# Kernel optimization log

Hardware: AMD Instinct MI355X
Metric: run time of the kernel (lower is better)

The kernel has to match this reference:

```python
import jax, jax.numpy as jnp
import numpy as np

B, N, D_MODEL = 16, 65536, 512
NBUCKETS = 11
BN_EPS = 1e-5
LN_EPS = 1e-5


def setup_inputs() -> dict:
    key = jax.random.key(0)
    ks = jax.random.split(key, 12)
    def w(k, shape, fan_in):
        return jax.random.normal(k, shape, jnp.float32) * (1.0 / np.sqrt(fan_in))
    return {
        "x": jax.random.normal(ks[0], (B, N, 3), jnp.float32),
        "w1": w(ks[1], (3, 64), 3),   "b1": jnp.zeros((64,), jnp.float32),
        "g1": jnp.ones((64,), jnp.float32),  "be1": jnp.zeros((64,), jnp.float32),
        "w2": w(ks[2], (64, 128), 64), "b2": jnp.zeros((128,), jnp.float32),
        "g2": jnp.ones((128,), jnp.float32), "be2": jnp.zeros((128,), jnp.float32),
        "w3": w(ks[3], (128, 256), 128), "b3": jnp.zeros((256,), jnp.float32),
        "g3": jnp.ones((256,), jnp.float32), "be3": jnp.zeros((256,), jnp.float32),
        "wp": w(ks[4], (518, D_MODEL), 518), "bp": jnp.zeros((D_MODEL,), jnp.float32),
        "g_ln": jnp.ones((D_MODEL,), jnp.float32), "b_ln": jnp.zeros((D_MODEL,), jnp.float32),
    }


def _bn(h, g, b):
    # BatchNorm1d in training mode: biased variance over the flattened batch axis
    m = jnp.mean(h, axis=0)
    v = jnp.mean((h - m) ** 2, axis=0)
    return (h - m) * jax.lax.rsqrt(v + BN_EPS) * g + b


def reference(x, w1, b1, g1, be1, w2, b2, g2, be2, w3, b3, g3, be3, wp, bp, g_ln, b_ln):
    Bb, Nn, _ = x.shape
    x_flat = x.reshape(Bb * Nn, 3)
    h = jax.nn.relu(_bn(x_flat @ w1 + b1, g1, be1))
    h = jax.nn.relu(_bn(h @ w2 + b2, g2, be2))
    h = jax.nn.relu(_bn(h @ w3 + b3, g3, be3))
    feat = h.reshape(Bb, Nn, 256)

    # y-bucket histogram means of (x, z) coordinates, vectorized via segment_sum
    y = x[:, :, 1]
    y_min = jnp.min(y, axis=1, keepdims=True)
    y_max = jnp.max(y, axis=1, keepdims=True)
    y_norm = (y - y_min) / (y_max - y_min + 1e-6)
    buckets = jnp.clip((y_norm * 10).astype(jnp.int32), 0, NBUCKETS - 1)  # (B,N) in [0,10]
    seg = (jnp.arange(Bb, dtype=jnp.int32)[:, None] * NBUCKETS + buckets).reshape(-1)
    nseg = Bb * NBUCKETS
    sx = jax.ops.segment_sum(x[:, :, 0].reshape(-1), seg, num_segments=nseg)
    sz = jax.ops.segment_sum(x[:, :, 2].reshape(-1), seg, num_segments=nseg)
    cnt = jax.ops.segment_sum(jnp.ones((Bb * Nn,), jnp.float32), seg, num_segments=nseg)
    denom = jnp.maximum(cnt, 1.0)
    cx = (sx / denom).reshape(Bb, NBUCKETS)
    cz = (sz / denom).reshape(Bb, NBUCKETS)
    x_centers = jnp.take_along_axis(cx, buckets, axis=1)  # (B,N)
    z_centers = jnp.take_along_axis(cz, buckets, axis=1)

    dx = x[:, :, 0] - x_centers
    dz = x[:, :, 2] - z_centers
    theta = jnp.arctan2(dz, dx)
    r = jnp.sqrt(dx ** 2 + dz ** 2)
    spatial = jnp.stack([jnp.sin(theta), jnp.cos(theta), r], axis=-1)  # (B,N,3)

    feat = jnp.concatenate([feat, spatial], axis=-1)  # (B,N,259)
    feat_max = jnp.max(feat, axis=1)
    feat_avg = jnp.mean(feat, axis=1)
    feat_cat = jnp.concatenate([feat_max, feat_avg], axis=1)  # (B,518)

    out = feat_cat @ wp + bp
    mu = jnp.mean(out, axis=-1, keepdims=True)
    var = jnp.mean((out - mu) ** 2, axis=-1, keepdims=True)
    return (out - mu) * jax.lax.rsqrt(var + LN_EPS) * g_ln + b_ln
```

## Files before the change

### kernel.cpp

```cpp
#include <hip/hip_runtime.h>
#include <stdint.h>

#define B_    16
#define N_    65536
#define NPTS  (B_*N_)
#define NBK   11
#define NFEAT 259
#define NF    ((float)NPTS)

typedef float f32x4 __attribute__((ext_vector_type(4)));
typedef short s16x8 __attribute__((ext_vector_type(8)));

enum {
  OFF_YMINF = 16,
  OFF_YMAXF = 32,
  OFF_A1    = 64,
  OFF_C1    = 128,
  OFF_A2    = 192,
  OFF_C2    = 320,
  OFF_CX    = 448,
  OFF_CZ    = 624,
  OFF_A3    = 800,
  OFF_C3    = 1056,
  OFF_PSTR  = 16384,
  OFF_PBKT  = 24576,
  OFF_PH2   = 49152,
  OFF_PH3   = 180224,
  OFF_PPOOL = 442368,
  OFF_PSPA  = 704512
};

__device__ __forceinline__ float wave_sum(float v){
  #pragma unroll
  for (int m=32;m>=1;m>>=1) v += __shfl_xor(v,m,64);
  return v;
}
__device__ __forceinline__ float wave_max(float v){
  #pragma unroll
  for (int m=32;m>=1;m>>=1) v = fmaxf(v,__shfl_xor(v,m,64));
  return v;
}
__device__ __forceinline__ float wave_min(float v){
  #pragma unroll
  for (int m=32;m>=1;m>>=1) v = fminf(v,__shfl_xor(v,m,64));
  return v;
}
__device__ __forceinline__ unsigned short bf16_bits(float f){
  unsigned u=__float_as_uint(f);
  u += 0x7FFFu + ((u>>16)&1u);
  return (unsigned short)(u>>16);
}

__global__ __launch_bounds__(256) void k_stream0(const float* __restrict__ x,
                                                 float* __restrict__ ws){
  __shared__ float red[4][12];
  const int t=threadIdx.x, l=t&63, w=t>>6;
  const int bid=blockIdx.x;
  const float4* xv=(const float4*)(x + (size_t)bid*2048*3);
  float s0=0,s1=0,s2=0,q00=0,q01=0,q02=0,q11=0,q12=0,q22=0;
  float ymn=3.4e38f, ymx=-3.4e38f;
  #pragma unroll
  for (int i=0;i<2;i++){
    const int vi=(i*256+t)*3;
    const float4 a=xv[vi], b4=xv[vi+1], c=xv[vi+2];
    float X[4]={a.x,a.w,b4.z,c.y};
    float Y[4]={a.y,b4.x,b4.w,c.z};
    float Z[4]={a.z,b4.y,c.x,c.w};
    #pragma unroll
    for (int p=0;p<4;p++){
      s0+=X[p]; s1+=Y[p]; s2+=Z[p];
      q00=fmaf(X[p],X[p],q00); q01=fmaf(X[p],Y[p],q01); q02=fmaf(X[p],Z[p],q02);
      q11=fmaf(Y[p],Y[p],q11); q12=fmaf(Y[p],Z[p],q12); q22=fmaf(Z[p],Z[p],q22);
      ymn=fminf(ymn,Y[p]); ymx=fmaxf(ymx,Y[p]);
    }
  }
  s0=wave_sum(s0); s1=wave_sum(s1); s2=wave_sum(s2);
  q00=wave_sum(q00); q01=wave_sum(q01); q02=wave_sum(q02);
  q11=wave_sum(q11); q12=wave_sum(q12); q22=wave_sum(q22);
  ymn=wave_min(ymn); ymx=wave_max(ymx);
  if (l==0){
    red[w][0]=s0; red[w][1]=s1; red[w][2]=s2;
    red[w][3]=q00; red[w][4]=q01; red[w][5]=q02;
    red[w][6]=q11; red[w][7]=q12; red[w][8]=q22;
    red[w][9]=ymn; red[w][10]=ymx;
  }
  __syncthreads();
  if (t<11){
    const float v0=red[0][t],v1=red[1][t],v2=red[2][t],v3=red[3][t];
    float r;
    if (t==9)       r=fminf(fminf(v0,v1),fminf(v2,v3));
    else if (t==10) r=fmaxf(fmaxf(v0,v1),fmaxf(v2,v3));
    else            r=v0+v1+v2+v3;
    ws[OFF_PSTR+bid*16+t]=r;
  }
}

__global__ void k_finA(const float* __restrict__ w1, const float* __restrict__ b1,
                       const float* __restrict__ gm, const float* __restrict__ bt,
                       float* __restrict__ ws){
  __shared__ float sums[9];
  const int t=threadIdx.x;
  if (t<9){
    float s=0.f;
    #pragma unroll 8
    for (int blk=0;blk<512;blk++) s+=ws[OFF_PSTR+blk*16+t];
    sums[t]=s;
  }
  if (t>=32&&t<48){
    const int b=t-32; float m=3.4e38f;
    #pragma unroll 8
    for (int blk=0;blk<32;blk++) m=fminf(m,ws[OFF_PSTR+(b*32+blk)*16+9]);
    ws[OFF_YMINF+b]=m;
  }
  if (t>=48&&t<64){
    const int b=t-48; float m=-3.4e38f;
    #pragma unroll 8
    for (int blk=0;blk<32;blk++) m=fmaxf(m,ws[OFF_PSTR+(b*32+blk)*16+10]);
    ws[OFF_YMAXF+b]=m;
  }
  __syncthreads();
  if (t<64){
    const float i_n=1.f/NF;
    const float w0=w1[t], wa=w1[64+t], wb=w1[128+t];
    const float ms=(w0*sums[0]+wa*sums[1]+wb*sums[2])*i_n;
    const float es=(w0*w0*sums[3]+wa*wa*sums[6]+wb*wb*sums[8]
                   +2.f*(w0*wa*sums[4]+w0*wb*sums[5]+wa*wb*sums[7]))*i_n;
    const float var=es-ms*ms;
    const float a=gm[t]/sqrtf(var+1e-5f);
    ws[OFF_A1+t]=a; ws[OFF_C1+t]=bt[t]-(ms+b1[t])*a;
  }
}

__global__ __launch_bounds__(256) void k_bucket(const float* __restrict__ x,
                                                float* __restrict__ ws){
  __shared__ float red[4][33];
  const int t=threadIdx.x, l=t&63, w=t>>6;
  const int bid=blockIdx.x, b=bid>>5;
  const float ymn=ws[OFF_YMINF+b], ymx=ws[OFF_YMAXF+b];
  const float4* xv=(const float4*)(x + (size_t)bid*2048*3);
  float sxl[NBK], szl[NBK], cntl[NBK];
  #pragma unroll
  for (int k=0;k<NBK;k++){ sxl[k]=0.f; szl[k]=0.f; cntl[k]=0.f; }
  #pragma unroll
  for (int i=0;i<2;i++){
    const int vi=(i*256+t)*3;
    const float4 a=xv[vi], b4=xv[vi+1], c=xv[vi+2];
    float X[4]={a.x,a.w,b4.z,c.y};
    float Y[4]={a.y,b4.x,b4.w,c.z};
    float Z[4]={a.z,b4.y,c.x,c.w};
    #pragma unroll
    for (int p=0;p<4;p++){
      const float yn=(Y[p]-ymn)/(ymx-ymn+1e-6f);
      int bk=(int)(yn*10.f); bk = bk<0?0:(bk>10?10:bk);
      #pragma unroll
      for (int k=0;k<NBK;k++){
        const bool m=(bk==k);
        sxl[k]+= m?X[p]:0.f; szl[k]+= m?Z[p]:0.f; cntl[k]+= m?1.f:0.f;
      }
    }
  }
  #pragma unroll
  for (int k=0;k<NBK;k++){
    const float s=wave_sum(sxl[k]);
    const float z=wave_sum(szl[k]);
    const float c=wave_sum(cntl[k]);
    if (l==0){ red[w][k]=s; }
    __syncthreads();
    if (l==0&&w==0){  }
    __syncthreads();
    if (l==0){ red[w][k]=s; }
    if (l==0){ red[w][k]=s; }
    __syncthreads();
    if (t<1){}
    if (l==0){ red[w][k]=s; }
    (void)z; (void)c;
    break;
  }
  #pragma unroll
  for (int k=0;k<NBK;k++){
    const float s=wave_sum(sxl[k]);
    if (l==0) red[w][k]=s;
  }
  __syncthreads();
  if (t<NBK) ws[OFF_PBKT+bid*36+t]=red[0][t]+red[1][t]+red[2][t]+red[3][t];
  __syncthreads();
  #pragma unroll
  for (int k=0;k<NBK;k++){
    const float z=wave_sum(szl[k]);
    if (l==0) red[w][k]=z;
  }
  __syncthreads();
  if (t<NBK) ws[OFF_PBKT+bid*36+11+t]=red[0][t]+red[1][t]+red[2][t]+red[3][t];
  __syncthreads();
  #pragma unroll
  for (int k=0;k<NBK;k++){
    const float c=wave_sum(cntl[k]);
    if (l==0) red[w][k]=c;
  }
  __syncthreads();
  if (t<NBK) ws[OFF_PBKT+bid*36+22+t]=red[0][t]+red[1][t]+red[2][t]+red[3][t];
}

__global__ void k_finB(const float* __restrict__ gm, const float* __restrict__ bt,
                       float* __restrict__ ws){
  __shared__ float acc[256];
  const int t=threadIdx.x;
  {
    const int col=t&127, part=t>>7;
    float s=0.f;
    #pragma unroll 8
    for (int blk=0;blk<512;blk++) s+=ws[OFF_PH2+blk*256+part*128+col];
    acc[t]=s;
  }
  __syncthreads();
  if (t<128){
    const float i_n=1.f/NF;
    const float m=acc[t]*i_n;
    const float v=acc[128+t]*i_n-m*m;
    const float a=gm[t]/sqrtf(v+1e-5f);
    ws[OFF_A2+t]=a; ws[OFF_C2+t]=bt[t]-m*a;
  }
  if (t<176){
    const int b=t/NBK, k=t-b*NBK;
    float sx=0.f, sz=0.f, cn=0.f;
    #pragma unroll 8
    for (int blk=0;blk<32;blk++){
      const int p=OFF_PBKT+(b*32+blk)*36;
      sx+=ws[p+k]; sz+=ws[p+11+k]; cn+=ws[p+22+k];
    }
    const float d=fmaxf(cn,1.f);
    ws[OFF_CX+t]=sx/d; ws[OFF_CZ+t]=sz/d;
  }
}

__global__ void k_finC(const float* __restrict__ gm, const float* __restrict__ bt,
                       float* __restrict__ ws){
  __shared__ float acc[512];
  const int t=threadIdx.x;
  {
    const int col=t&255, part=t>>8;
    float s=0.f;
    #pragma unroll 8
    for (int blk=0;blk<512;blk++) s+=ws[OFF_PH3+blk*512+part*256+col];
    acc[t]=s;
  }
  __syncthreads();
  if (t<256){
    const float i_n=1.f/NF;
    const float m=acc[t]*i_n;
    const float v=acc[256+t]*i_n-m*m;
    const float a=gm[t]/sqrtf(v+1e-5f);
    ws[OFF_A3+t]=a; ws[OFF_C3+t]=bt[t]-m*a;
  }
}

__global__ __launch_bounds__(256) void k_spatial(const float* __restrict__ x,
                                                 float* __restrict__ ws){
  __shared__ float red[4][8];
  const int t=threadIdx.x, l=t&63, w=t>>6;
  const int bid=blockIdx.x, b=bid>>5;
  const float ymn=ws[OFF_YMINF+b], ymx=ws[OFF_YMAXF+b];
  const float4* xv=(const float4*)(x + (size_t)bid*2048*3);
  float mx[3]={-3.4e38f,-3.4e38f,-3.4e38f}, sm[3]={0.f,0.f,0.f};
  #pragma unroll
  for (int i=0;i<2;i++){
    const int vi=(i*256+t)*3;
    const float4 a=xv[vi], b4=xv[vi+1], c=xv[vi+2];
    float X[4]={a.x,a.w,b4.z,c.y};
    float Y[4]={a.y,b4.x,b4.w,c.z};
    float Z[4]={a.z,b4.y,c.x,c.w};
    #pragma unroll
    for (int p=0;p<4;p++){
      const float yn=(Y[p]-ymn)/(ymx-ymn+1e-6f);
      int bk=(int)(yn*10.f); bk = bk<0?0:(bk>10?10:bk);
      const float dx=X[p]-ws[OFF_CX+b*NBK+bk];
      const float dz=Z[p]-ws[OFF_CZ+b*NBK+bk];
      const float r=sqrtf(fmaf(dx,dx,dz*dz));
      const float sn=(r>0.f)?(dz/r):0.f;
      const float cs=(r>0.f)?(dx/r):1.f;
      mx[0]=fmaxf(mx[0],sn); sm[0]+=sn;
      mx[1]=fmaxf(mx[1],cs); sm[1]+=cs;
      mx[2]=fmaxf(mx[2],r);  sm[2]+=r;
    }
  }
  #pragma unroll
  for (int q=0;q<3;q++){
    const float m=wave_max(mx[q]);
    const float s=wave_sum(sm[q]);
    if (l==0){ red[w][q]=m; red[w][4+q]=s; }
  }
  __syncthreads();
  if (t<3)        ws[OFF_PSPA+bid*8+t]  =fmaxf(fmaxf(red[0][t],red[1][t]),fmaxf(red[2][t],red[3][t]));
  else if (t>=4&&t<7){
    const int q=t-4;
    ws[OFF_PSPA+bid*8+4+q]=red[0][4+q]+red[1][4+q]+red[2][4+q]+red[3][4+q];
  }
}

template<int MODE>
__global__ __launch_bounds__(256,2) void k_mlp(
    const float* __restrict__ x,
    const float* __restrict__ w1, const float* __restrict__ b1,
    const float* __restrict__ w2, const float* __restrict__ b2,
    const float* __restrict__ w3, const float* __restrict__ b3,
    float* __restrict__ ws)
{
  __shared__ short g1t[64*64];
  __shared__ short g2t[64*128];
  const int t=threadIdx.x, w=t>>6, l=t&63, lg=l>>4, lr=l&15;
  const int b=blockIdx.x>>5, chunk=blockIdx.x&31;
  const int bid=blockIdx.x;

  const float* a1=ws+OFF_A1; const float* c1=ws+OFF_C1;
  float w1A[3][8], w1B[3][8], b1A[8], b1B[8];
  #pragma unroll
  for (int i=0;i<8;i++){
    const int fA=8*lg+i, fB=32+8*lg+i;
    const float aA=a1[fA], aB=a1[fB];
    #pragma unroll
    for (int q=0;q<3;q++){ w1A[q][i]=w1[q*64+fA]*aA; w1B[q][i]=w1[q*64+fB]*aB; }
    b1A[i]=b1[fA]*aA+c1[fA];
    b1B[i]=b1[fB]*aB+c1[fB];
  }

  s16x8 w2f[2][2]; float b2v[2];
  #pragma unroll
  for (int ct=0;ct<2;ct++){
    const int col=(2*w+ct)*16+lr;
    const float sc=(MODE==0)?1.f:ws[OFF_A2+col];
    b2v[ct]=(MODE==0)? b2[col] : (ws[OFF_A2+col]*b2[col]+ws[OFF_C2+col]);
    #pragma unroll
    for (int kt=0;kt<2;kt++){
      #pragma unroll
      for (int i=0;i<8;i++){
        const int k=kt*32+8*lg+i;
        w2f[ct][kt][i]=(short)bf16_bits(w2[k*128+col]*sc);
      }
    }
  }

  s16x8 w3f[4][4]; float b3v[4]={0,0,0,0};
  if (MODE!=0){
    #pragma unroll
    for (int ct=0;ct<4;ct++){
      const int col=(4*w+ct)*16+lr;
      const float sc=(MODE==1)?1.f:ws[OFF_A3+col];
      b3v[ct]=(MODE==1)? b3[col] : (ws[OFF_A3+col]*b3[col]+ws[OFF_C3+col]);
      #pragma unroll
      for (int kt=0;kt<4;kt++){
        #pragma unroll
        for (int i=0;i<8;i++){
          const int k=kt*32+8*lg+i;
          w3f[ct][kt][i]=(short)bf16_bits(w3[k*256+col]*sc);
        }
      }
    }
  }

  float accS[4], accQ[4]={0.f,0.f,0.f,0.f};
  #pragma unroll
  for (int q_=0;q_<4;q_++) accS[q_]=(MODE==2)?-3.4e38f:0.f;

  char* g1c=(char*)g1t; char* g2c=(char*)g2t;

  for (int it=0; it<32; ++it){
    const int tb=b*N_+chunk*2048+it*64;
    {
      const int p=16*w+lr;
      const float x0=x[(tb+p)*3+0], x1=x[(tb+p)*3+1], x2=x[(tb+p)*3+2];
      float h[8]; unsigned pk[4];
      #pragma unroll
      for (int i=0;i<8;i++){
        float v=b1A[i];
        v=fmaf(x0,w1A[0][i],v); v=fmaf(x1,w1A[1][i],v); v=fmaf(x2,w1A[2][i],v);
        h[i]=fmaxf(v,0.f);
      }
      #pragma unroll
      for (int i=0;i<4;i++) pk[i]=(unsigned)bf16_bits(h[2*i]) | ((unsigned)bf16_bits(h[2*i+1])<<16);
      *(int4*)(g1c + (((p*64+8*lg)*2) ^ ((p&7)<<4))) = make_int4(pk[0],pk[1],pk[2],pk[3]);
      #pragma unroll
      for (int i=0;i<8;i++){
        float v=b1B[i];
        v=fmaf(x0,w1B[0][i],v); v=fmaf(x1,w1B[1][i],v); v=fmaf(x2,w1B[2][i],v);
        h[i]=fmaxf(v,0.f);
      }
      #pragma unroll
      for (int i=0;i<4;i++) pk[i]=(unsigned)bf16_bits(h[2*i]) | ((unsigned)bf16_bits(h[2*i+1])<<16);
      *(int4*)(g1c + (((p*64+32+8*lg)*2) ^ ((p&7)<<4))) = make_int4(pk[0],pk[1],pk[2],pk[3]);
    }
    __syncthreads();
    s16x8 a1f[4][2];
    #pragma unroll
    for (int rt=0;rt<4;rt++){
      const int p=rt*16+lr;
      #pragma unroll
      for (int kt=0;kt<2;kt++)
        a1f[rt][kt]=*(const s16x8*)(g1c + (((p*64+kt*32+8*lg)*2) ^ ((p&7)<<4)));
    }
    #pragma unroll
    for (int ct=0;ct<2;ct++){
      const int col=(2*w+ct)*16+lr;
      #pragma unroll
      for (int rt=0;rt<4;rt++){
        f32x4 acc={0.f,0.f,0.f,0.f};
        acc=__builtin_amdgcn_mfma_f32_16x16x32_bf16(a1f[rt][0],w2f[ct][0],acc,0,0,0);
        acc=__builtin_amdgcn_mfma_f32_16x16x32_bf16(a1f[rt][1],w2f[ct][1],acc,0,0,0);
        if (MODE==0){
          #pragma unroll
          for (int r=0;r<4;r++){ const float h2=acc[r]+b2v[ct]; accS[ct]+=h2; accQ[ct]+=h2*h2; }
        } else {
          #pragma unroll
          for (int r=0;r<4;r++){
            const int p=rt*16+4*lg+r;
            const float g=fmaxf(acc[r]+b2v[ct],0.f);
            *(short*)(g2c + (((p*128+col)*2) ^ ((p&7)<<4))) = (short)bf16_bits(g);
          }
        }
      }
    }
    __syncthreads();
    if (MODE!=0){
      #pragma unroll
      for (int rt=0;rt<4;rt++){
        const int p=rt*16+lr;
        s16x8 a2f[4];
        #pragma unroll
        for (int kt=0;kt<4;kt++)
          a2f[kt]=*(const s16x8*)(g2c + (((p*128+kt*32+8*lg)*2) ^ ((p&7)<<4)));
        #pragma unroll
        for (int ct=0;ct<4;ct++){
          f32x4 acc={0.f,0.f,0.f,0.f};
          #pragma unroll
          for (int kt=0;kt<4;kt++)
            acc=__builtin_amdgcn_mfma_f32_16x16x32_bf16(a2f[kt],w3f[ct][kt],acc,0,0,0);
          #pragma unroll
          for (int r=0;r<4;r++){
            if (MODE==1){ const float h3=acc[r]+b3v[ct]; accS[ct]+=h3; accQ[ct]+=h3*h3; }
            else        { const float g=fmaxf(acc[r]+b3v[ct],0.f); accS[ct]=fmaxf(accS[ct],g); accQ[ct]+=g; }
          }
        }
      }
    }
  }

  if (MODE==0){
    #pragma unroll
    for (int ct=0;ct<2;ct++){
      float s=accS[ct], q=accQ[ct];
      s+=__shfl_xor(s,16); s+=__shfl_xor(s,32);
      q+=__shfl_xor(q,16); q+=__shfl_xor(q,32);
      if (l<16){
        const int col=(2*w+ct)*16+lr;
        ws[OFF_PH2+bid*256+col]    =s;
        ws[OFF_PH2+bid*256+128+col]=q;
      }
    }
  } else if (MODE==1){
    #pragma unroll
    for (int ct=0;ct<4;ct++){
      float s=accS[ct], q=accQ[ct];
      s+=__shfl_xor(s,16); s+=__shfl_xor(s,32);
      q+=__shfl_xor(q,16); q+=__shfl_xor(q,32);
      if (l<16){
        const int col=(4*w+ct)*16+lr;
        ws[OFF_PH3+bid*512+col]    =s;
        ws[OFF_PH3+bid*512+256+col]=q;
      }
    }
  } else {
    #pragma unroll
    for (int ct=0;ct<4;ct++){
      float m=accS[ct], s=accQ[ct];
      m=fmaxf(m,__shfl_xor(m,16)); m=fmaxf(m,__shfl_xor(m,32));
      s+=__shfl_xor(s,16); s+=__shfl_xor(s,32);
      if (l<16){
        const int col=(4*w+ct)*16+lr;
        ws[OFF_PPOOL+bid*512+col]    =m;
        ws[OFF_PPOOL+bid*512+256+col]=s;
      }
    }
  }
}

__global__ __launch_bounds__(256) void k_final(
    const float* __restrict__ wp, const float* __restrict__ bp,
    const float* __restrict__ gln, const float* __restrict__ bln,
    float* __restrict__ out, const float* __restrict__ ws)
{
  __shared__ float feat[518];
  __shared__ float red[256];
  const int b=blockIdx.x, t=threadIdx.x;
  {
    float fm=-3.4e38f, fs=0.f;
    #pragma unroll 4
    for (int blk=0;blk<32;blk++){
      const int p=OFF_PPOOL+(b*32+blk)*512;
      fm=fmaxf(fm,ws[p+t]);
      fs+=ws[p+256+t];
    }
    feat[t]=fm; feat[NFEAT+t]=fs*(1.f/65536.f);
  }
  if (t<3){
    float fm=-3.4e38f, fs=0.f;
    #pragma unroll 4
    for (int blk=0;blk<32;blk++){
      const int p=OFF_PSPA+(b*32+blk)*8;
      fm=fmaxf(fm,ws[p+t]);
      fs+=ws[p+4+t];
    }
    feat[256+t]=fm; feat[NFEAT+256+t]=fs*(1.f/65536.f);
  }
  __syncthreads();
  float o0=bp[t], o1=bp[t+256];
  #pragma unroll 4
  for (int i=0;i<518;i++){
    const float f=feat[i];
    o0=fmaf(f, wp[i*512+t],     o0);
    o1=fmaf(f, wp[i*512+t+256], o1);
  }
  red[t]=o0+o1; __syncthreads();
  for (int s=128;s>0;s>>=1){ if (t<s) red[t]+=red[t+s]; __syncthreads(); }
  const float mu=red[0]*(1.f/512.f);
  __syncthreads();
  const float d0=o0-mu, d1=o1-mu;
  red[t]=d0*d0+d1*d1; __syncthreads();
  for (int s=128;s>0;s>>=1){ if (t<s) red[t]+=red[t+s]; __syncthreads(); }
  const float var=red[0]*(1.f/512.f);
  const float rs=1.f/sqrtf(var+1e-5f);
  out[b*512+t]     = d0*rs*gln[t]    +bln[t];
  out[b*512+t+256] = d1*rs*gln[t+256]+bln[t+256];
}

extern "C" void kernel_launch(void* const* d_in, const int* in_sizes, int n_in,
                              void* d_out, int out_size, void* d_ws, size_t ws_size,
                              hipStream_t stream)
{
  const float* x  =(const float*)d_in[0];
  const float* w1 =(const float*)d_in[1];
  const float* b1 =(const float*)d_in[2];
  const float* gm1=(const float*)d_in[3];
  const float* be1=(const float*)d_in[4];
  const float* w2 =(const float*)d_in[5];
  const float* b2 =(const float*)d_in[6];
  const float* gm2=(const float*)d_in[7];
  const float* be2=(const float*)d_in[8];
  const float* w3 =(const float*)d_in[9];
  const float* b3 =(const float*)d_in[10];
  const float* gm3=(const float*)d_in[11];
  const float* be3=(const float*)d_in[12];
  const float* wp =(const float*)d_in[13];
  const float* bp =(const float*)d_in[14];
  const float* gln=(const float*)d_in[15];
  const float* bln=(const float*)d_in[16];
  float* ws=(float*)d_ws;
  float* out=(float*)d_out;

  k_stream0<<<dim3(512),dim3(256),0,stream>>>(x,ws);
  k_finA   <<<dim3(1),  dim3(256),0,stream>>>(w1,b1,gm1,be1,ws);
  k_bucket <<<dim3(512),dim3(256),0,stream>>>(x,ws);
  k_mlp<0> <<<dim3(512),dim3(256),0,stream>>>(x,w1,b1,w2,b2,w3,b3,ws);
  k_finB   <<<dim3(1),  dim3(256),0,stream>>>(gm2,be2,ws);
  k_spatial<<<dim3(512),dim3(256),0,stream>>>(x,ws);
  k_mlp<1> <<<dim3(512),dim3(256),0,stream>>>(x,w1,b1,w2,b2,w3,b3,ws);
  k_finC   <<<dim3(1),  dim3(512),0,stream>>>(gm3,be3,ws);
  k_mlp<2> <<<dim3(512),dim3(256),0,stream>>>(x,w1,b1,w2,b2,w3,b3,ws);
  k_final  <<<dim3(16), dim3(256),0,stream>>>(wp,bp,gln,bln,out,ws);
}
```

Before: 486.5 us.

## Restructure MLP kernel to 8 waves with transposed MFMA operands and fewer registers

The MLP kernel moves from 256 to 512 threads per block. Each wave now owns fewer output columns, and the MFMA operands are swapped so that weights are the A operand and activations the B operand. The per-thread weight fragments and accumulators shrink, which should allow four blocks per CU and more parallelism. Layer-2 outputs are written to LDS as packed 8-byte stores instead of scalar shorts, and the final reduction becomes a 16-lane shuffle. The dead reduction loop with redundant syncthreads in k_bucket is removed. The trade-off is more barrier participants per block and a longer shuffle reduction at the end.

```diff
diff --git a/kernel.cpp b/kernel.cpp
--- a/kernel.cpp
+++ b/kernel.cpp
@@ -133,7 +133,7 @@
 
 __global__ __launch_bounds__(256) void k_bucket(const float* __restrict__ x,
                                                 float* __restrict__ ws){
-  __shared__ float red[4][33];
+  __shared__ float red[4][12];
   const int t=threadIdx.x, l=t&63, w=t>>6;
   const int bid=blockIdx.x, b=bid>>5;
   const float ymn=ws[OFF_YMINF+b], ymx=ws[OFF_YMAXF+b];
@@ -158,23 +158,6 @@
         sxl[k]+= m?X[p]:0.f; szl[k]+= m?Z[p]:0.f; cntl[k]+= m?1.f:0.f;
       }
     }
-  }
-  #pragma unroll
-  for (int k=0;k<NBK;k++){
-    const float s=wave_sum(sxl[k]);
-    const float z=wave_sum(szl[k]);
-    const float c=wave_sum(cntl[k]);
-    if (l==0){ red[w][k]=s; }
-    __syncthreads();
-    if (l==0&&w==0){  }
-    __syncthreads();
-    if (l==0){ red[w][k]=s; }
-    if (l==0){ red[w][k]=s; }
-    __syncthreads();
-    if (t<1){}
-    if (l==0){ red[w][k]=s; }
-    (void)z; (void)c;
-    break;
   }
   #pragma unroll
   for (int k=0;k<NBK;k++){
@@ -298,7 +281,7 @@
 }
 
 template<int MODE>
-__global__ __launch_bounds__(256,2) void k_mlp(
+__global__ __launch_bounds__(512,4) void k_mlp(
     const float* __restrict__ x,
     const float* __restrict__ w1, const float* __restrict__ b1,
     const float* __restrict__ w2, const float* __restrict__ b2,
@@ -308,135 +291,130 @@
   __shared__ short g1t[64*64];
   __shared__ short g2t[64*128];
   const int t=threadIdx.x, w=t>>6, l=t&63, lg=l>>4, lr=l&15;
-  const int b=blockIdx.x>>5, chunk=blockIdx.x&31;
-  const int bid=blockIdx.x;
-
+  const int bid=blockIdx.x, b=bid>>5, chunk=bid&31;
+
+  const int p1=8*w+(l&7), fg=l>>3&7;
   const float* a1=ws+OFF_A1; const float* c1=ws+OFF_C1;
-  float w1A[3][8], w1B[3][8], b1A[8], b1B[8];
+  float w1f[3][8], b1f[8];
   #pragma unroll
   for (int i=0;i<8;i++){
-    const int fA=8*lg+i, fB=32+8*lg+i;
-    const float aA=a1[fA], aB=a1[fB];
-    #pragma unroll
-    for (int q=0;q<3;q++){ w1A[q][i]=w1[q*64+fA]*aA; w1B[q][i]=w1[q*64+fB]*aB; }
-    b1A[i]=b1[fA]*aA+c1[fA];
-    b1B[i]=b1[fB]*aB+c1[fB];
-  }
-
-  s16x8 w2f[2][2]; float b2v[2];
-  #pragma unroll
-  for (int ct=0;ct<2;ct++){
-    const int col=(2*w+ct)*16+lr;
-    const float sc=(MODE==0)?1.f:ws[OFF_A2+col];
-    b2v[ct]=(MODE==0)? b2[col] : (ws[OFF_A2+col]*b2[col]+ws[OFF_C2+col]);
-    #pragma unroll
-    for (int kt=0;kt<2;kt++){
-      #pragma unroll
-      for (int i=0;i<8;i++){
-        const int k=kt*32+8*lg+i;
-        w2f[ct][kt][i]=(short)bf16_bits(w2[k*128+col]*sc);
-      }
-    }
-  }
-
-  s16x8 w3f[4][4]; float b3v[4]={0,0,0,0};
+    const int f=8*fg+i;
+    const float a=a1[f];
+    #pragma unroll
+    for (int q=0;q<3;q++) w1f[q][i]=w1[q*64+f]*a;
+    b1f[i]=b1[f]*a+c1[f];
+  }
+
+  s16x8 w2f[2]; float b2v[4];
+  {
+    const int col2=16*w+lr;
+    const float sc2=(MODE==0)?1.f:ws[OFF_A2+col2];
+    #pragma unroll
+    for (int kt=0;kt<2;kt++)
+      #pragma unroll
+      for (int i=0;i<8;i++)
+        w2f[kt][i]=(short)bf16_bits(w2[(kt*32+8*lg+i)*128+col2]*sc2);
+    #pragma unroll
+    for (int r=0;r<4;r++){
+      const int f2=16*w+4*lg+r;
+      b2v[r]=(MODE==0)? b2[f2] : (ws[OFF_A2+f2]*b2[f2]+ws[OFF_C2+f2]);
+    }
+  }
+
+  s16x8 w3f[2][4]; float b3v[2][4];
   if (MODE!=0){
     #pragma unroll
-    for (int ct=0;ct<4;ct++){
-      const int col=(4*w+ct)*16+lr;
-      const float sc=(MODE==1)?1.f:ws[OFF_A3+col];
-      b3v[ct]=(MODE==1)? b3[col] : (ws[OFF_A3+col]*b3[col]+ws[OFF_C3+col]);
-      #pragma unroll
-      for (int kt=0;kt<4;kt++){
+    for (int ft=0;ft<2;ft++){
+      const int col3=(2*w+ft)*16+lr;
+      const float sc3=(MODE==1)?1.f:ws[OFF_A3+col3];
+      #pragma unroll
+      for (int kt=0;kt<4;kt++)
         #pragma unroll
-        for (int i=0;i<8;i++){
-          const int k=kt*32+8*lg+i;
-          w3f[ct][kt][i]=(short)bf16_bits(w3[k*256+col]*sc);
+        for (int i=0;i<8;i++)
+          w3f[ft][kt][i]=(short)bf16_bits(w3[(kt*32+8*lg+i)*256+col3]*sc3);
+      #pragma unroll
+      for (int r=0;r<4;r++){
+        const int f3=(2*w+ft)*16+4*lg+r;
+        b3v[ft][r]=(MODE==1)? b3[f3] : (ws[OFF_A3+f3]*b3[f3]+ws[OFF_C3+f3]);
+      }
+    }
+  }
+
+  float aS[2][4], aQ[2][4];
+  #pragma unroll
+  for (int ft=0;ft<2;ft++)
+    #pragma unroll
+    for (int r=0;r<4;r++){ aS[ft][r]=(MODE==2)?-3.4e38f:0.f; aQ[ft][r]=0.f; }
+
+  char* g1c=(char*)g1t; char* g2c=(char*)g2t;
+  const int base=b*N_+chunk*2048;
+
+  #pragma unroll 1
+  for (int it=0; it<32; ++it){
+    const int tb=base+it*64;
+    {
+      const float x0=x[(tb+p1)*3+0], x1v=x[(tb+p1)*3+1], x2=x[(tb+p1)*3+2];
+      unsigned pk[4];
+      #pragma unroll
+      for (int i=0;i<4;i++){
+        float v0=b1f[2*i],v1=b1f[2*i+1];
+        v0=fmaf(x0,w1f[0][2*i],v0);   v1=fmaf(x0,w1f[0][2*i+1],v1);
+        v0=fmaf(x1v,w1f[1][2*i],v0);  v1=fmaf(x1v,w1f[1][2*i+1],v1);
+        v0=fmaf(x2,w1f[2][2*i],v0);   v1=fmaf(x2,w1f[2][2*i+1],v1);
+        v0=fmaxf(v0,0.f); v1=fmaxf(v1,0.f);
+        pk[i]=(unsigned)bf16_bits(v0)|((unsigned)bf16_bits(v1)<<16);
+      }
+      *(int4*)(g1c + ((p1*128+fg*16) ^ ((p1&7)<<4))) = make_int4(pk[0],pk[1],pk[2],pk[3]);
+    }
+    __syncthreads();
+    #pragma unroll
+    for (int pt=0;pt<4;pt++){
+      const int p=pt*16+lr;
+      s16x8 bf[2];
+      #pragma unroll
+      for (int kt=0;kt<2;kt++)
+        bf[kt]=*(const s16x8*)(g1c + ((p*128+kt*64+16*lg) ^ ((p&7)<<4)));
+      f32x4 acc={0.f,0.f,0.f,0.f};
+      acc=__builtin_amdgcn_mfma_f32_16x16x32_bf16(w2f[0],bf[0],acc,0,0,0);
+      acc=__builtin_amdgcn_mfma_f32_16x16x32_bf16(w2f[1],bf[1],acc,0,0,0);
+      if (MODE==0){
+        #pragma unroll
+        for (int r=0;r<4;r++){
+          const float h=acc[r]+b2v[r];
+          aS[0][r]+=h; aQ[0][r]+=h*h;
         }
-      }
-    }
-  }
-
-  float accS[4], accQ[4]={0.f,0.f,0.f,0.f};
-  #pragma unroll
-  for (int q_=0;q_<4;q_++) accS[q_]=(MODE==2)?-3.4e38f:0.f;
-
-  char* g1c=(char*)g1t; char* g2c=(char*)g2t;
-
-  for (int it=0; it<32; ++it){
-    const int tb=b*N_+chunk*2048+it*64;
-    {
-      const int p=16*w+lr;
-      const float x0=x[(tb+p)*3+0], x1=x[(tb+p)*3+1], x2=x[(tb+p)*3+2];
-      float h[8]; unsigned pk[4];
-      #pragma unroll
-      for (int i=0;i<8;i++){
-        float v=b1A[i];
-        v=fmaf(x0,w1A[0][i],v); v=fmaf(x1,w1A[1][i],v); v=fmaf(x2,w1A[2][i],v);
-        h[i]=fmaxf(v,0.f);
-      }
-      #pragma unroll
-      for (int i=0;i<4;i++) pk[i]=(unsigned)bf16_bits(h[2*i]) | ((unsigned)bf16_bits(h[2*i+1])<<16);
-      *(int4*)(g1c + (((p*64+8*lg)*2) ^ ((p&7)<<4))) = make_int4(pk[0],pk[1],pk[2],pk[3]);
-      #pragma unroll
-      for (int i=0;i<8;i++){
-        float v=b1B[i];
-        v=fmaf(x0,w1B[0][i],v); v=fmaf(x1,w1B[1][i],v); v=fmaf(x2,w1B[2][i],v);
-        h[i]=fmaxf(v,0.f);
-      }
-      #pragma unroll
-      for (int i=0;i<4;i++) pk[i]=(unsigned)bf16_bits(h[2*i]) | ((unsigned)bf16_bits(h[2*i+1])<<16);
-      *(int4*)(g1c + (((p*64+32+8*lg)*2) ^ ((p&7)<<4))) = make_int4(pk[0],pk[1],pk[2],pk[3]);
-    }
-    __syncthreads();
-    s16x8 a1f[4][2];
-    #pragma unroll
-    for (int rt=0;rt<4;rt++){
-      const int p=rt*16+lr;
-      #pragma unroll
-      for (int kt=0;kt<2;kt++)
-        a1f[rt][kt]=*(const s16x8*)(g1c + (((p*64+kt*32+8*lg)*2) ^ ((p&7)<<4)));
-    }
-    #pragma unroll
-    for (int ct=0;ct<2;ct++){
-      const int col=(2*w+ct)*16+lr;
-      #pragma unroll
-      for (int rt=0;rt<4;rt++){
-        f32x4 acc={0.f,0.f,0.f,0.f};
-        acc=__builtin_amdgcn_mfma_f32_16x16x32_bf16(a1f[rt][0],w2f[ct][0],acc,0,0,0);
-        acc=__builtin_amdgcn_mfma_f32_16x16x32_bf16(a1f[rt][1],w2f[ct][1],acc,0,0,0);
-        if (MODE==0){
-          #pragma unroll
-          for (int r=0;r<4;r++){ const float h2=acc[r]+b2v[ct]; accS[ct]+=h2; accQ[ct]+=h2*h2; }
-        } else {
-          #pragma unroll
-          for (int r=0;r<4;r++){
-            const int p=rt*16+4*lg+r;
-            const float g=fmaxf(acc[r]+b2v[ct],0.f);
-            *(short*)(g2c + (((p*128+col)*2) ^ ((p&7)<<4))) = (short)bf16_bits(g);
-          }
-        }
+      } else {
+        float g0=fmaxf(acc[0]+b2v[0],0.f), g1v=fmaxf(acc[1]+b2v[1],0.f);
+        float g2v=fmaxf(acc[2]+b2v[2],0.f), g3=fmaxf(acc[3]+b2v[3],0.f);
+        const unsigned lo=(unsigned)bf16_bits(g0)|((unsigned)bf16_bits(g1v)<<16);
+        const unsigned hi=(unsigned)bf16_bits(g2v)|((unsigned)bf16_bits(g3)<<16);
+        *(uint2*)(g2c + ((p*256+w*32+lg*8) ^ ((p&7)<<4))) = make_uint2(lo,hi);
       }
     }
     __syncthreads();
     if (MODE!=0){
       #pragma unroll
-      for (int rt=0;rt<4;rt++){
-        const int p=rt*16+lr;
-        s16x8 a2f[4];
+      for (int pt=0;pt<4;pt++){
+        const int p=pt*16+lr;
+        s16x8 bf[4];
         #pragma unroll
         for (int kt=0;kt<4;kt++)
-          a2f[kt]=*(const s16x8*)(g2c + (((p*128+kt*32+8*lg)*2) ^ ((p&7)<<4)));
+          bf[kt]=*(const s16x8*)(g2c + ((p*256+kt*64+16*lg) ^ ((p&7)<<4)));
         #pragma unroll
-        for (int ct=0;ct<4;ct++){
+        for (int ft=0;ft<2;ft++){
           f32x4 acc={0.f,0.f,0.f,0.f};
           #pragma unroll
           for (int kt=0;kt<4;kt++)
-            acc=__builtin_amdgcn_mfma_f32_16x16x32_bf16(a2f[kt],w3f[ct][kt],acc,0,0,0);
+            acc=__builtin_amdgcn_mfma_f32_16x16x32_bf16(w3f[ft][kt],bf[kt],acc,0,0,0);
           #pragma unroll
           for (int r=0;r<4;r++){
-            if (MODE==1){ const float h3=acc[r]+b3v[ct]; accS[ct]+=h3; accQ[ct]+=h3*h3; }
-            else        { const float g=fmaxf(acc[r]+b3v[ct],0.f); accS[ct]=fmaxf(accS[ct],g); accQ[ct]+=g; }
+            if (MODE==1){
+              const float h=acc[r]+b3v[ft][r];
+              aS[ft][r]+=h; aQ[ft][r]+=h*h;
+            } else {
+              const float g=fmaxf(acc[r]+b3v[ft][r],0.f);
+              aS[ft][r]=fmaxf(aS[ft][r],g); aQ[ft][r]+=g;
+            }
           }
         }
       }
@@ -445,40 +423,44 @@
 
   if (MODE==0){
     #pragma unroll
-    for (int ct=0;ct<2;ct++){
-      float s=accS[ct], q=accQ[ct];
-      s+=__shfl_xor(s,16); s+=__shfl_xor(s,32);
-      q+=__shfl_xor(q,16); q+=__shfl_xor(q,32);
-      if (l<16){
-        const int col=(2*w+ct)*16+lr;
-        ws[OFF_PH2+bid*256+col]    =s;
-        ws[OFF_PH2+bid*256+128+col]=q;
+    for (int r=0;r<4;r++){
+      float s=aS[0][r], q=aQ[0][r];
+      #pragma unroll
+      for (int m=1;m<16;m<<=1){ s+=__shfl_xor(s,m); q+=__shfl_xor(q,m); }
+      if (lr==0){
+        const int f2=16*w+4*lg+r;
+        ws[OFF_PH2+bid*256+f2]    =s;
+        ws[OFF_PH2+bid*256+128+f2]=q;
       }
     }
   } else if (MODE==1){
     #pragma unroll
-    for (int ct=0;ct<4;ct++){
-      float s=accS[ct], q=accQ[ct];
-      s+=__shfl_xor(s,16); s+=__shfl_xor(s,32);
-      q+=__shfl_xor(q,16); q+=__shfl_xor(q,32);
-      if (l<16){
-        const int col=(4*w+ct)*16+lr;
-        ws[OFF_PH3+bid*512+col]    =s;
-        ws[OFF_PH3+bid*512+256+col]=q;
-      }
-    }
+    for (int ft=0;ft<2;ft++)
+      #pragma unroll
+      for (int r=0;r<4;r++){
+        float s=aS[ft][r], q=aQ[ft][r];
+        #pragma unroll
+        for (int m=1;m<16;m<<=1){ s+=__shfl_xor(s,m); q+=__shfl_xor(q,m); }
+        if (lr==0){
+          const int f3=(2*w+ft)*16+4*lg+r;
+          ws[OFF_PH3+bid*512+f3]    =s;
+          ws[OFF_PH3+bid*512+256+f3]=q;
+        }
+      }
   } else {
     #pragma unroll
-    for (int ct=0;ct<4;ct++){
-      float m=accS[ct], s=accQ[ct];
-      m=fmaxf(m,__shfl_xor(m,16)); m=fmaxf(m,__shfl_xor(m,32));
-      s+=__shfl_xor(s,16); s+=__shfl_xor(s,32);
-      if (l<16){
-        const int col=(4*w+ct)*16+lr;
-        ws[OFF_PPOOL+bid*512+col]    =m;
-        ws[OFF_PPOOL+bid*512+256+col]=s;
-      }
-    }
+    for (int ft=0;ft<2;ft++)
+      #pragma unroll
+      for (int r=0;r<4;r++){
+        float mxv=aS[ft][r], s=aQ[ft][r];
+        #pragma unroll
+        for (int m=1;m<16;m<<=1){ mxv=fmaxf(mxv,__shfl_xor(mxv,m)); s+=__shfl_xor(s,m); }
+        if (lr==0){
+          const int f3=(2*w+ft)*16+4*lg+r;
+          ws[OFF_PPOOL+bid*512+f3]    =mxv;
+          ws[OFF_PPOOL+bid*512+256+f3]=s;
+        }
+      }
   }
 }
 
@@ -558,11 +540,11 @@
   k_stream0<<<dim3(512),dim3(256),0,stream>>>(x,ws);
   k_finA   <<<dim3(1),  dim3(256),0,stream>>>(w1,b1,gm1,be1,ws);
   k_bucket <<<dim3(512),dim3(256),0,stream>>>(x,ws);
-  k_mlp<0> <<<dim3(512),dim3(256),0,stream>>>(x,w1,b1,w2,b2,w3,b3,ws);
+  k_mlp<0> <<<dim3(512),dim3(512),0,stream>>>(x,w1,b1,w2,b2,w3,b3,ws);
   k_finB   <<<dim3(1),  dim3(256),0,stream>>>(gm2,be2,ws);
   k_spatial<<<dim3(512),dim3(256),0,stream>>>(x,ws);
-  k_mlp<1> <<<dim3(512),dim3(256),0,stream>>>(x,w1,b1,w2,b2,w3,b3,ws);
+  k_mlp<1> <<<dim3(512),dim3(512),0,stream>>>(x,w1,b1,w2,b2,w3,b3,ws);
   k_finC   <<<dim3(1),  dim3(512),0,stream>>>(gm3,be3,ws);
-  k_mlp<2> <<<dim3(512),dim3(256),0,stream>>>(x,w1,b1,w2,b2,w3,b3,ws);
+  k_mlp<2> <<<dim3(512),dim3(512),0,stream>>>(x,w1,b1,w2,b2,w3,b3,ws);
   k_final  <<<dim3(16), dim3(256),0,stream>>>(wp,bp,gln,bln,out,ws);
 }
```

Result: slower. 965.2 us (+98.4%).
